# Optimization experiments

Hardware: AMD Instinct MI355X
Metric: run time of the kernel (lower is better)

## Reference

```python
import jax, jax.numpy as jnp
import numpy as np

B, T, C, H = 16, 2048, 1024, 64

def setup_inputs() -> dict:
    key = jax.random.key(0)
    kx, kq, kk, kv = jax.random.split(key, 4)
    x = jax.random.normal(kx, (B, T, C), dtype=jnp.float32)
    Wq = jax.random.normal(kq, (C, H), dtype=jnp.float32) * (C ** -0.5)
    Wk = jax.random.normal(kk, (C, H), dtype=jnp.float32) * (C ** -0.5)
    Wv = jax.random.normal(kv, (C, H), dtype=jnp.float32) * (C ** -0.5)
    return {"x": x, "Wq": Wq, "Wk": Wk, "Wv": Wv}

def reference(x, Wq, Wk, Wv):
    # single causal self-attention head; dropout p=0.0 (identity)
    Tlen = x.shape[1]
    q = jnp.einsum('btc,ch->bth', x, Wq)  # [B,T,H]
    k = jnp.einsum('btc,ch->bth', x, Wk)
    v = jnp.einsum('btc,ch->bth', x, Wv)
    scale = q.shape[-1] ** -0.5
    scores = jnp.einsum('bth,bsh->bts', q, k) * scale  # [B,T,T]
    causal = jnp.tril(jnp.ones((Tlen, Tlen), dtype=bool))
    scores = jnp.where(causal, scores, -jnp.inf)
    weights = jax.nn.softmax(scores, axis=-1)
    out = jnp.einsum('bts,bsh->bth', weights, v)  # [B,T,H]
    return out
```

## Files before the change

### kernel.cpp

```cpp
#include <hip/hip_runtime.h>


typedef float  floatx4 __attribute__((ext_vector_type(4)));
typedef __bf16 bf16x8  __attribute__((ext_vector_type(8)));
typedef unsigned short ushort4v __attribute__((ext_vector_type(4)));
typedef unsigned int   uint2v   __attribute__((ext_vector_type(2)));
typedef unsigned int   uint4v   __attribute__((ext_vector_type(4)));

constexpr int Bn = 16;
constexpr int Tn = 2048;
constexpr int Cn = 1024;
constexpr int Hn = 64;
constexpr int BT = Bn * Tn;

constexpr float QSCALE = 0.125f * 1.44269504088896340736f;

__device__ __forceinline__ unsigned short f2b(float f) {
  unsigned int u = __builtin_bit_cast(unsigned int, f);
  u += 0x7fffu + ((u >> 16) & 1u);
  return (unsigned short)(u >> 16);
}

__device__ __forceinline__ unsigned int cvt_pk_bf16(float lo, float hi) {
  unsigned int r;
  asm("v_cvt_pk_bf16_f32 %0, %1, %2" : "=v"(r) : "v"(lo), "v"(hi));
  return r;
}

__global__ __launch_bounds__(256) void pack_w(const float* __restrict__ Wq,
                                              const float* __restrict__ Wk,
                                              const float* __restrict__ Wv,
                                              unsigned short* __restrict__ Wp) {
  int gid = blockIdx.x * 256 + threadIdx.x;
  int mat = gid >> 16;
  int rem = gid & 65535;
  int k   = rem >> 6;
  int col = rem & 63;
  const float* W = (mat == 0) ? Wq : (mat == 1) ? Wk : Wv;
  float v = W[rem];
  int kb = k >> 3, j = k & 7, ct = (mat << 2) | (col >> 4), c = col & 15;
  size_t idx = ((((size_t)ct * 128) + kb) * 16 + c) * 8 + j;
  Wp[idx] = f2b(v);
}

__global__ __launch_bounds__(256) void proj_kernel(
    const float* __restrict__ x, const unsigned short* __restrict__ Wp,
    unsigned short* __restrict__ Q, unsigned short* __restrict__ K,
    unsigned short* __restrict__ Vt) {
  __shared__ alignas(16) unsigned short Bl[12 * 1024];

  const int tid  = threadIdx.x;
  const int wave = tid >> 6;
  const int lane = tid & 63;
  const int quad = lane >> 4;
  const int l16  = lane & 15;
  const int wr   = wave >> 1;
  const int wc   = wave & 1;
  const int rbase = blockIdx.x * 64;

  floatx4 acc[2][6];
#pragma unroll
  for (int a = 0; a < 2; ++a)
#pragma unroll
    for (int b = 0; b < 6; ++b) acc[a][b] = (floatx4){0.f, 0.f, 0.f, 0.f};

  const float* xp = x + (size_t)(rbase + wr * 32 + l16) * Cn + quad * 8;

  for (int k0 = 0; k0 < Cn; k0 += 64) {
    floatx4 fa[2][2][2];
#pragma unroll
    for (int rg = 0; rg < 2; ++rg) {
      const float* bp = xp + rg * 16 * Cn + k0;
      fa[rg][0][0] = *reinterpret_cast<const floatx4*>(bp);
      fa[rg][0][1] = *reinterpret_cast<const floatx4*>(bp + 4);
      fa[rg][1][0] = *reinterpret_cast<const floatx4*>(bp + 32);
      fa[rg][1][1] = *reinterpret_cast<const floatx4*>(bp + 36);
    }

    if (k0) __syncthreads();

#pragma unroll
    for (int i = 0; i < 3; ++i) {
      const int ct = wave * 3 + i;
#pragma unroll
      for (int h = 0; h < 2; ++h) {
        const unsigned short* g =
            Wp + ((size_t)(ct * 128 + (k0 >> 3) + h * 4 + quad) * 16 + l16) * 8;
        __builtin_amdgcn_global_load_lds(
            (const __attribute__((address_space(1))) void*)g,
            (__attribute__((address_space(3))) void*)&Bl[ct * 1024 + h * 512],
            16, 0, 0);
      }
    }

    bf16x8 af[2][2];
#pragma unroll
    for (int rg = 0; rg < 2; ++rg)
#pragma unroll
      for (int kk = 0; kk < 2; ++kk) {
        uint4v u;
        u[0] = cvt_pk_bf16(fa[rg][kk][0][0], fa[rg][kk][0][1]);
        u[1] = cvt_pk_bf16(fa[rg][kk][0][2], fa[rg][kk][0][3]);
        u[2] = cvt_pk_bf16(fa[rg][kk][1][0], fa[rg][kk][1][1]);
        u[3] = cvt_pk_bf16(fa[rg][kk][1][2], fa[rg][kk][1][3]);
        af[rg][kk] = __builtin_bit_cast(bf16x8, u);
      }

    __syncthreads();

#pragma unroll
    for (int kk = 0; kk < 2; ++kk) {
#pragma unroll
      for (int c6 = 0; c6 < 6; ++c6) {
        const int ct = wc * 6 + c6;
        bf16x8 bfr = *reinterpret_cast<const bf16x8*>(
            &Bl[ct * 1024 + (kk * 4 + quad) * 128 + l16 * 8]);
        acc[0][c6] = __builtin_amdgcn_mfma_f32_16x16x32_bf16(af[0][kk], bfr, acc[0][c6], 0, 0, 0);
        acc[1][c6] = __builtin_amdgcn_mfma_f32_16x16x32_bf16(af[1][kk], bfr, acc[1][c6], 0, 0, 0);
      }
    }
  }

#pragma unroll
  for (int rt = 0; rt < 2; ++rt) {
#pragma unroll
    for (int c6 = 0; c6 < 6; ++c6) {
      const int cbase  = wc * 96 + c6 * 16;
      const int rowloc = wr * 32 + rt * 16 + quad * 4;
      if (cbase < 64) {
#pragma unroll
        for (int r = 0; r < 4; ++r)
          Q[(size_t)(rbase + rowloc + r) * Hn + cbase + l16] =
              f2b(acc[rt][c6][r] * QSCALE);
      } else if (cbase < 128) {
#pragma unroll
        for (int r = 0; r < 4; ++r)
          K[(size_t)(rbase + rowloc + r) * Hn + cbase - 64 + l16] =
              f2b(acc[rt][c6][r]);
      } else {
        const int b  = rbase >> 11;
        const int t0 = (rbase & 2047) + rowloc;
        const int h  = cbase - 128 + l16;
        ushort4v v;
#pragma unroll
        for (int r = 0; r < 4; ++r) v[r] = f2b(acc[rt][c6][r]);
        *reinterpret_cast<ushort4v*>(&Vt[((size_t)b * Hn + h) * Tn + t0]) = v;
      }
    }
  }
}

__global__ __launch_bounds__(256) void flash_kernel(
    const unsigned short* __restrict__ Q, const unsigned short* __restrict__ K,
    const unsigned short* __restrict__ Vt, float* __restrict__ out) {
  __shared__ alignas(16) unsigned short P[4][16][64];
  __shared__ alignas(16) float Om[4][16][68];
  __shared__ float Ml[4][16][2];

  const int tid  = threadIdx.x;
  const int wave = tid >> 6;
  const int lane = tid & 63;
  const int quad = lane >> 4;
  const int l16  = lane & 15;

  const int b   = blockIdx.x & 15;
  const int p16 = 127 - (blockIdx.x >> 4);
  const int qbase = p16 * 16;
  const int n_tiles  = (p16 >> 2) + 1;
  const int lastTile = p16 >> 2;
  const size_t bbase  = (size_t)b * Tn * Hn;
  const size_t vtbase = (size_t)b * Hn * Tn;

  bf16x8 qf[2];
#pragma unroll
  for (int i = 0; i < 2; ++i)
    qf[i] = *reinterpret_cast<const bf16x8*>(
        &Q[bbase + (size_t)(qbase + l16) * Hn + i * 32 + quad * 8]);

  floatx4 O[4];
#pragma unroll
  for (int i = 0; i < 4; ++i) O[i] = (floatx4){0.f, 0.f, 0.f, 0.f};
  float m_r = -INFINITY, l_r = 0.f;

  const int swz  = (l16 & 7) << 3;
  const int trow = qbase + l16;

  for (int kt = wave; kt < n_tiles; kt += 4) {
    const int kvbase = kt * 64;

    floatx4 S[4];
    __builtin_amdgcn_s_setprio(1);
#pragma unroll
    for (int ct = 0; ct < 4; ++ct) {
      floatx4 s = (floatx4){0.f, 0.f, 0.f, 0.f};
#pragma unroll
      for (int kk = 0; kk < 2; ++kk) {
        bf16x8 kf = *reinterpret_cast<const bf16x8*>(
            &K[bbase + (size_t)(kvbase + ct * 16 + l16) * Hn + kk * 32 + quad * 8]);
        s = __builtin_amdgcn_mfma_f32_16x16x32_bf16(kf, qf[kk], s, 0, 0, 0);
      }
      S[ct] = s;
    }
    __builtin_amdgcn_s_setprio(0);

    bf16x8 vf[4][2];
#pragma unroll
    for (int ht = 0; ht < 4; ++ht)
#pragma unroll
      for (int kk = 0; kk < 2; ++kk)
        vf[ht][kk] = *reinterpret_cast<const bf16x8*>(
            &Vt[vtbase + (size_t)(ht * 16 + l16) * Tn + kvbase + kk * 32 + quad * 8]);

    if (kt == lastTile) {
#pragma unroll
      for (int ct = 0; ct < 4; ++ct)
#pragma unroll
        for (int r = 0; r < 4; ++r)
          if (kvbase + ct * 16 + quad * 4 + r > trow) S[ct][r] = -1e30f;
    }

    float mx0 = fmaxf(fmaxf(S[0][0], S[0][1]), fmaxf(S[0][2], S[0][3]));
    float mx1 = fmaxf(fmaxf(S[1][0], S[1][1]), fmaxf(S[1][2], S[1][3]));
    float mx2 = fmaxf(fmaxf(S[2][0], S[2][1]), fmaxf(S[2][2], S[2][3]));
    float mx3 = fmaxf(fmaxf(S[3][0], S[3][1]), fmaxf(S[3][2], S[3][3]));
    float mx  = fmaxf(fmaxf(mx0, mx1), fmaxf(mx2, mx3));
    mx = fmaxf(mx, __shfl_xor(mx, 16));
    mx = fmaxf(mx, __shfl_xor(mx, 32));
    float mnew  = fmaxf(m_r, mx);
    float alpha = __builtin_amdgcn_exp2f(m_r - mnew);
    float rs = 0.f;
#pragma unroll
    for (int ct = 0; ct < 4; ++ct)
#pragma unroll
      for (int r = 0; r < 4; ++r) {
        float p = __builtin_amdgcn_exp2f(S[ct][r] - mnew);
        S[ct][r] = p;
        rs += p;
      }
    rs += __shfl_xor(rs, 16);
    rs += __shfl_xor(rs, 32);
    l_r = l_r * alpha + rs;
    m_r = mnew;
#pragma unroll
    for (int ht = 0; ht < 4; ++ht)
#pragma unroll
      for (int r = 0; r < 4; ++r) O[ht][r] *= alpha;

#pragma unroll
    for (int ct = 0; ct < 4; ++ct) {
      uint2v w;
      w[0] = cvt_pk_bf16(S[ct][0], S[ct][1]);
      w[1] = cvt_pk_bf16(S[ct][2], S[ct][3]);
      *reinterpret_cast<uint2v*>(&P[wave][l16][(ct * 16 + quad * 4) ^ swz]) = w;
    }
    bf16x8 pf0 = *reinterpret_cast<const bf16x8*>(&P[wave][l16][(quad * 8) ^ swz]);
    bf16x8 pf1 = *reinterpret_cast<const bf16x8*>(&P[wave][l16][(32 + quad * 8) ^ swz]);

    __builtin_amdgcn_s_setprio(1);
#pragma unroll
    for (int ht = 0; ht < 4; ++ht) {
      O[ht] = __builtin_amdgcn_mfma_f32_16x16x32_bf16(vf[ht][0], pf0, O[ht], 0, 0, 0);
      O[ht] = __builtin_amdgcn_mfma_f32_16x16x32_bf16(vf[ht][1], pf1, O[ht], 0, 0, 0);
    }
    __builtin_amdgcn_s_setprio(0);
  }

#pragma unroll
  for (int ht = 0; ht < 4; ++ht)
#pragma unroll
    for (int r = 0; r < 4; ++r)
      Om[wave][l16][ht * 16 + quad * 4 + r] = O[ht][r];
  if (quad == 0) {
    Ml[wave][l16][0] = m_r;
    Ml[wave][l16][1] = l_r;
  }
  __syncthreads();

  {
    const int row = tid >> 4;
    const int c4  = (tid & 15) * 4;
    float m0 = Ml[0][row][0], m1 = Ml[1][row][0];
    float m2 = Ml[2][row][0], m3 = Ml[3][row][0];
    float M = fmaxf(fmaxf(m0, m1), fmaxf(m2, m3));
    float e0 = __builtin_amdgcn_exp2f(m0 - M), e1 = __builtin_amdgcn_exp2f(m1 - M);
    float e2 = __builtin_amdgcn_exp2f(m2 - M), e3 = __builtin_amdgcn_exp2f(m3 - M);
    float L = Ml[0][row][1] * e0 + Ml[1][row][1] * e1 +
              Ml[2][row][1] * e2 + Ml[3][row][1] * e3;
    float invL = 1.0f / L;
    floatx4 o0 = *reinterpret_cast<const floatx4*>(&Om[0][row][c4]);
    floatx4 o1 = *reinterpret_cast<const floatx4*>(&Om[1][row][c4]);
    floatx4 o2 = *reinterpret_cast<const floatx4*>(&Om[2][row][c4]);
    floatx4 o3 = *reinterpret_cast<const floatx4*>(&Om[3][row][c4]);
    floatx4 res;
#pragma unroll
    for (int j = 0; j < 4; ++j)
      res[j] = (o0[j] * e0 + o1[j] * e1 + o2[j] * e2 + o3[j] * e3) * invL;
    *reinterpret_cast<floatx4*>(
        &out[bbase + (size_t)(qbase + row) * Hn + c4]) = res;
  }
}

extern "C" void kernel_launch(void* const* d_in, const int* in_sizes, int n_in,
                              void* d_out, int out_size, void* d_ws, size_t ws_size,
                              hipStream_t stream) {
  const float* x  = (const float*)d_in[0];
  const float* Wq = (const float*)d_in[1];
  const float* Wk = (const float*)d_in[2];
  const float* Wv = (const float*)d_in[3];
  float* out = (float*)d_out;

  char* ws = (char*)d_ws;
  unsigned short* Q  = (unsigned short*)(ws);
  unsigned short* Kb = (unsigned short*)(ws + ((size_t)4 << 20));
  unsigned short* Vt = (unsigned short*)(ws + ((size_t)8 << 20));
  unsigned short* Wp = (unsigned short*)(ws + ((size_t)12 << 20));

  pack_w<<<dim3(768), dim3(256), 0, stream>>>(Wq, Wk, Wv, Wp);
  proj_kernel<<<dim3(BT / 64), dim3(256), 0, stream>>>(x, Wp, Q, Kb, Vt);
  flash_kernel<<<dim3(16 * 128), dim3(256), 0, stream>>>(Q, Kb, Vt, out);
}
```

Baseline: 275.6 us.

## Double-buffer weight tiles in projection and defer softmax rescale in attention

The projection kernel now keeps two LDS buffers for the weight tiles and prefetches the next x and W tile while computing the current one, with one barrier per stage instead of two. Launch bounds request two blocks per SM. In the attention kernel, V loads are issued before the QK MFMAs, and the running-max rescale of O and l only happens when the max increases. This aims to hide global-load latency and skip redundant rescale work, at the cost of twice the LDS and possible register pressure or wave divergence on the rescale branch.

```diff
diff --git a/kernel.cpp b/kernel.cpp
--- a/kernel.cpp
+++ b/kernel.cpp
@@ -43,11 +43,11 @@
   Wp[idx] = f2b(v);
 }
 
-__global__ __launch_bounds__(256) void proj_kernel(
+__global__ __launch_bounds__(256, 2) void proj_kernel(
     const float* __restrict__ x, const unsigned short* __restrict__ Wp,
     unsigned short* __restrict__ Q, unsigned short* __restrict__ K,
     unsigned short* __restrict__ Vt) {
-  __shared__ alignas(16) unsigned short Bl[12 * 1024];
+  __shared__ alignas(16) unsigned short Bl[2][12 * 1024];
 
   const int tid  = threadIdx.x;
   const int wave = tid >> 6;
@@ -66,8 +66,25 @@
 
   const float* xp = x + (size_t)(rbase + wr * 32 + l16) * Cn + quad * 8;
 
-  for (int k0 = 0; k0 < Cn; k0 += 64) {
-    floatx4 fa[2][2][2];
+  auto stageB = [&](int t, int buf) {
+    const int kb0 = t << 3;
+#pragma unroll
+    for (int i = 0; i < 3; ++i) {
+      const int ct = wave * 3 + i;
+#pragma unroll
+      for (int h = 0; h < 2; ++h) {
+        const unsigned short* g =
+            Wp + ((size_t)(ct * 128 + kb0 + h * 4 + quad) * 16 + l16) * 8;
+        __builtin_amdgcn_global_load_lds(
+            (const __attribute__((address_space(1))) void*)g,
+            (__attribute__((address_space(3))) void*)&Bl[buf][ct * 1024 + h * 512],
+            16, 0, 0);
+      }
+    }
+  };
+
+  auto loadX = [&](int t, floatx4 (&fa)[2][2][2]) {
+    const int k0 = t * 64;
 #pragma unroll
     for (int rg = 0; rg < 2; ++rg) {
       const float* bp = xp + rg * 16 * Cn + k0;
@@ -76,23 +93,9 @@
       fa[rg][1][0] = *reinterpret_cast<const floatx4*>(bp + 32);
       fa[rg][1][1] = *reinterpret_cast<const floatx4*>(bp + 36);
     }
-
-    if (k0) __syncthreads();
-
-#pragma unroll
-    for (int i = 0; i < 3; ++i) {
-      const int ct = wave * 3 + i;
-#pragma unroll
-      for (int h = 0; h < 2; ++h) {
-        const unsigned short* g =
-            Wp + ((size_t)(ct * 128 + (k0 >> 3) + h * 4 + quad) * 16 + l16) * 8;
-        __builtin_amdgcn_global_load_lds(
-            (const __attribute__((address_space(1))) void*)g,
-            (__attribute__((address_space(3))) void*)&Bl[ct * 1024 + h * 512],
-            16, 0, 0);
-      }
-    }
-
+  };
+
+  auto compute = [&](const floatx4 (&fa)[2][2][2], int buf) {
     bf16x8 af[2][2];
 #pragma unroll
     for (int rg = 0; rg < 2; ++rg)
@@ -105,20 +108,37 @@
         u[3] = cvt_pk_bf16(fa[rg][kk][1][2], fa[rg][kk][1][3]);
         af[rg][kk] = __builtin_bit_cast(bf16x8, u);
       }
-
-    __syncthreads();
-
 #pragma unroll
     for (int kk = 0; kk < 2; ++kk) {
 #pragma unroll
       for (int c6 = 0; c6 < 6; ++c6) {
         const int ct = wc * 6 + c6;
         bf16x8 bfr = *reinterpret_cast<const bf16x8*>(
-            &Bl[ct * 1024 + (kk * 4 + quad) * 128 + l16 * 8]);
+            &Bl[buf][ct * 1024 + (kk * 4 + quad) * 128 + l16 * 8]);
         acc[0][c6] = __builtin_amdgcn_mfma_f32_16x16x32_bf16(af[0][kk], bfr, acc[0][c6], 0, 0, 0);
         acc[1][c6] = __builtin_amdgcn_mfma_f32_16x16x32_bf16(af[1][kk], bfr, acc[1][c6], 0, 0, 0);
       }
     }
+  };
+
+  floatx4 fa0[2][2][2], fa1[2][2][2];
+
+  stageB(0, 0);
+  loadX(0, fa0);
+  __syncthreads();
+
+  for (int tt = 0; tt < 8; ++tt) {
+    const int tb = tt * 2 + 1;
+    stageB(tb, 1);
+    loadX(tb, fa1);
+    compute(fa0, 0);
+    __syncthreads();
+    if (tb + 1 < 16) {
+      stageB(tb + 1, 0);
+      loadX(tb + 1, fa0);
+    }
+    compute(fa1, 1);
+    __syncthreads();
   }
 
 #pragma unroll
@@ -188,6 +208,14 @@
   for (int kt = wave; kt < n_tiles; kt += 4) {
     const int kvbase = kt * 64;
 
+    bf16x8 vf[4][2];
+#pragma unroll
+    for (int ht = 0; ht < 4; ++ht)
+#pragma unroll
+      for (int kk = 0; kk < 2; ++kk)
+        vf[ht][kk] = *reinterpret_cast<const bf16x8*>(
+            &Vt[vtbase + (size_t)(ht * 16 + l16) * Tn + kvbase + kk * 32 + quad * 8]);
+
     floatx4 S[4];
     __builtin_amdgcn_s_setprio(1);
 #pragma unroll
@@ -202,14 +230,6 @@
       S[ct] = s;
     }
     __builtin_amdgcn_s_setprio(0);
-
-    bf16x8 vf[4][2];
-#pragma unroll
-    for (int ht = 0; ht < 4; ++ht)
-#pragma unroll
-      for (int kk = 0; kk < 2; ++kk)
-        vf[ht][kk] = *reinterpret_cast<const bf16x8*>(
-            &Vt[vtbase + (size_t)(ht * 16 + l16) * Tn + kvbase + kk * 32 + quad * 8]);
 
     if (kt == lastTile) {
 #pragma unroll
@@ -226,25 +246,27 @@
     float mx  = fmaxf(fmaxf(mx0, mx1), fmaxf(mx2, mx3));
     mx = fmaxf(mx, __shfl_xor(mx, 16));
     mx = fmaxf(mx, __shfl_xor(mx, 32));
-    float mnew  = fmaxf(m_r, mx);
-    float alpha = __builtin_amdgcn_exp2f(m_r - mnew);
+    if (mx > m_r) {
+      float alpha = __builtin_amdgcn_exp2f(m_r - mx);
+      l_r *= alpha;
+#pragma unroll
+      for (int ht = 0; ht < 4; ++ht)
+#pragma unroll
+        for (int r = 0; r < 4; ++r) O[ht][r] *= alpha;
+      m_r = mx;
+    }
     float rs = 0.f;
 #pragma unroll
     for (int ct = 0; ct < 4; ++ct)
 #pragma unroll
       for (int r = 0; r < 4; ++r) {
-        float p = __builtin_amdgcn_exp2f(S[ct][r] - mnew);
+        float p = __builtin_amdgcn_exp2f(S[ct][r] - m_r);
         S[ct][r] = p;
         rs += p;
       }
     rs += __shfl_xor(rs, 16);
     rs += __shfl_xor(rs, 32);
-    l_r = l_r * alpha + rs;
-    m_r = mnew;
-#pragma unroll
-    for (int ht = 0; ht < 4; ++ht)
-#pragma unroll
-      for (int r = 0; r < 4; ++r) O[ht][r] *= alpha;
+    l_r += rs;
 
 #pragma unroll
     for (int ct = 0; ct < 4; ++ct) {
```

Measured after the change: 276.2 us. No clear change (+0.2%).
